# Optimization experiments

Measured on AMD Instinct MI355X. Metric: run time of the kernel, lower is better.

## Reference

```python
import jax, jax.numpy as jnp
import numpy as np

COMMISSION_RATIO = 0.0025
INTEREST_RATE = 0.00008
B, N = 4096, 8192


def setup_inputs() -> dict:
    key = jax.random.key(0)
    k1, k2 = jax.random.split(key)
    w = jax.random.uniform(k1, (B, 1, N), dtype=jnp.float32)
    w = w / jnp.sum(w, axis=-1, keepdims=True)  # portfolio weights sum to 1
    # price relatives close to 1 so log(reward) stays finite
    y = 1.0 + 0.02 * jax.random.normal(k2, (B, N, 1), dtype=jnp.float32)
    return {"w": w, "y": y}


def reference(w, y):
    # reward[b] = w[b] @ y[b]  -> [B,1,1]
    reward = jnp.einsum('bin,bnj->bij', w, y)
    # torch .view(B, 1, N) on contiguous [B, N, 1] == transpose here
    close_price = jnp.swapaxes(y, 1, 2)                     # [B,1,N]
    element_reward = w * close_price                        # [B,1,N]
    # interest: only negative elements contribute
    interest = jnp.sum(jnp.minimum(element_reward, 0.0), axis=2,
                       keepdims=True) * INTEREST_RATE       # [B,1,1]
    future_omega = element_reward / reward                  # [B,1,N]
    wt, wt1 = future_omega[:-1], w[1:]
    pure_pc = 1.0 - jnp.sum(jnp.abs(wt - wt1), axis=-1) * COMMISSION_RATIO  # [B-1,1]
    pure_pc = jnp.concatenate(
        [jnp.ones((1, 1), dtype=pure_pc.dtype), pure_pc], axis=0)  # [B,1]
    pure_pc = pure_pc[:, :, None]                           # [B,1,1]
    reward = reward * pure_pc + interest                    # [B,1,1]

    sr_reward = reward - 1.0
    SR = jnp.mean(sr_reward) / jnp.std(sr_reward, ddof=1)   # torch std is unbiased

    # max drawdown: cumprod of per-step changes, running max, relative dip
    pc = reward.reshape(-1)                                 # [B]
    pv = jnp.cumprod(pc)
    running_max = jax.lax.cummax(pv)
    MDD = jnp.max(1.0 - pv / running_max)

    portfolio_value = jnp.prod(reward, axis=0)              # [1,1]
    loss = -jnp.mean(jnp.log(reward))
    return loss, portfolio_value, SR, MDD
```

## Files before the change

kernel.cpp:

```cpp
#include <hip/hip_runtime.h>
#include <math.h>

#define B_DIM 4096
#define N_DIM 8192
#define K_ROWS 4
#define NBLK (B_DIM / K_ROWS)

__constant__ const float kCommission = 0.0025f;
__constant__ const float kInterest   = 8e-05f;

__global__ __launch_bounds__(256) void fused_reward_kernel(const float* __restrict__ w,
                                                           const float* __restrict__ y,
                                                           float* __restrict__ reward_out) {
    const int s    = blockIdx.x * K_ROWS;
    const int tid  = threadIdx.x;
    const int lane = tid & 63, wave = tid >> 6;
    __shared__ float red[4][3];

    float4 e_prev[8];
    #pragma unroll
    for (int j = 0; j < 8; ++j) e_prev[j] = make_float4(0.f, 0.f, 0.f, 0.f);
    float inv_dprev = 0.f;

    if (s > 0) {
        const float4* wp = (const float4*)(w + (size_t)(s - 1) * N_DIM);
        const float4* yp = (const float4*)(y + (size_t)(s - 1) * N_DIM);
        float4 wv[8], yv[8];
        #pragma unroll
        for (int j = 0; j < 8; ++j) wv[j] = wp[tid + 256 * j];
        #pragma unroll
        for (int j = 0; j < 8; ++j) yv[j] = yp[tid + 256 * j];
        float d = 0.f;
        #pragma unroll
        for (int j = 0; j < 8; ++j) {
            float4 ev;
            ev.x = wv[j].x * yv[j].x; ev.y = wv[j].y * yv[j].y;
            ev.z = wv[j].z * yv[j].z; ev.w = wv[j].w * yv[j].w;
            d += (ev.x + ev.y) + (ev.z + ev.w);
            e_prev[j] = ev;
        }
        #pragma unroll
        for (int off = 32; off; off >>= 1) d += __shfl_down(d, off);
        if (lane == 0) red[wave][0] = d;
        __syncthreads();
        float dot_prev = (red[0][0] + red[1][0]) + (red[2][0] + red[3][0]);
        inv_dprev = 1.0f / dot_prev;
        __syncthreads();
    }

    #pragma unroll 1
    for (int k = 0; k < K_ROWS; ++k) {
        const int r = s + k;
        const float4* wp = (const float4*)(w + (size_t)r * N_DIM);
        const float4* yp = (const float4*)(y + (size_t)r * N_DIM);
        float4 wv[8], yv[8];
        #pragma unroll
        for (int j = 0; j < 8; ++j) wv[j] = wp[tid + 256 * j];
        #pragma unroll
        for (int j = 0; j < 8; ++j) yv[j] = yp[tid + 256 * j];

        float d = 0.f, it = 0.f, cm = 0.f;
        #pragma unroll
        for (int j = 0; j < 8; ++j) {
            float4 ev;
            ev.x = wv[j].x * yv[j].x; ev.y = wv[j].y * yv[j].y;
            ev.z = wv[j].z * yv[j].z; ev.w = wv[j].w * yv[j].w;
            d  += (ev.x + ev.y) + (ev.z + ev.w);
            it += (fminf(ev.x, 0.f) + fminf(ev.y, 0.f)) +
                  (fminf(ev.z, 0.f) + fminf(ev.w, 0.f));
            cm += (fabsf(fmaf(e_prev[j].x, inv_dprev, -wv[j].x)) +
                   fabsf(fmaf(e_prev[j].y, inv_dprev, -wv[j].y))) +
                  (fabsf(fmaf(e_prev[j].z, inv_dprev, -wv[j].z)) +
                   fabsf(fmaf(e_prev[j].w, inv_dprev, -wv[j].w)));
            e_prev[j] = ev;
        }
        #pragma unroll
        for (int off = 32; off; off >>= 1) {
            d  += __shfl_down(d,  off);
            it += __shfl_down(it, off);
            cm += __shfl_down(cm, off);
        }
        if (lane == 0) { red[wave][0] = d; red[wave][1] = it; red[wave][2] = cm; }
        __syncthreads();
        const float dot_r = (red[0][0] + red[1][0]) + (red[2][0] + red[3][0]);
        const float int_r = ((red[0][1] + red[1][1]) + (red[2][1] + red[3][1])) * kInterest;
        const float comm  = (red[0][2] + red[1][2]) + (red[2][2] + red[3][2]);
        const float pc = (r == 0) ? 1.0f : fmaf(-comm, kCommission, 1.0f);
        if (tid == 0) reward_out[r] = dot_r * pc + int_r;
        inv_dprev = 1.0f / dot_r;
        __syncthreads();
    }
}

__global__ __launch_bounds__(1024) void finalize_kernel(const float* __restrict__ reward,
                                                        float* __restrict__ out) {
    const int T = 1024, PER = B_DIM / T;
    const int tid = threadIdx.x;
    const int lane = tid & 63, wave = tid >> 6;

    float r[PER], lc[PER];
    float csum = 0.f;
    #pragma unroll
    for (int j = 0; j < PER; ++j) {
        r[j] = reward[tid * PER + j];
        csum += logf(r[j]);
        lc[j] = csum;
    }

    float v = csum;
    #pragma unroll
    for (int off = 1; off < 64; off <<= 1) {
        float t = __shfl_up(v, off);
        if (lane >= off) v += t;
    }
    __shared__ float wsum[16];
    __shared__ float woff[17];
    if (lane == 63) wsum[wave] = v;
    __syncthreads();
    if (tid == 0) {
        float acc = 0.f;
        for (int i = 0; i < 16; ++i) { woff[i] = acc; acc += wsum[i]; }
        woff[16] = acc;
    }
    __syncthreads();
    float ev = __shfl_up(v, 1);
    if (lane == 0) ev = 0.f;
    const float excl = woff[wave] + ev;
    float S[PER];
    #pragma unroll
    for (int j = 0; j < PER; ++j) S[j] = excl + lc[j];
    const float total_logs = woff[16];

    float rm = -INFINITY;
    float cmax[PER];
    #pragma unroll
    for (int j = 0; j < PER; ++j) { rm = fmaxf(rm, S[j]); cmax[j] = rm; }
    float mv = rm;
    #pragma unroll
    for (int off = 1; off < 64; off <<= 1) {
        float t = __shfl_up(mv, off);
        if (lane >= off) mv = fmaxf(mv, t);
    }
    __shared__ float wmax[16];
    __shared__ float wmoff[16];
    if (lane == 63) wmax[wave] = mv;
    __syncthreads();
    if (tid == 0) {
        float acc = -INFINITY;
        for (int i = 0; i < 16; ++i) { wmoff[i] = acc; acc = fmaxf(acc, wmax[i]); }
    }
    __syncthreads();
    float emv = __shfl_up(mv, 1);
    if (lane == 0) emv = -INFINITY;
    const float mexcl = fmaxf(wmoff[wave], emv);

    float ddmax = 0.f;
    #pragma unroll
    for (int j = 0; j < PER; ++j) {
        float M = fmaxf(mexcl, cmax[j]);
        ddmax = fmaxf(ddmax, 1.0f - expf(S[j] - M));
    }
    #pragma unroll
    for (int off = 32; off; off >>= 1) ddmax = fmaxf(ddmax, __shfl_down(ddmax, off));
    __shared__ float wdd[16];
    if (lane == 0) wdd[wave] = ddmax;

    double sr_ = 0.0;
    #pragma unroll
    for (int j = 0; j < PER; ++j) sr_ += (double)r[j];
    #pragma unroll
    for (int off = 32; off; off >>= 1) sr_ += __shfl_down(sr_, off);
    __shared__ double wsr[16];
    if (lane == 0) wsr[wave] = sr_;
    __syncthreads();
    __shared__ double mean_sh;
    if (tid == 0) {
        double sm = 0.0;
        for (int i = 0; i < 16; ++i) sm += wsr[i];
        mean_sh = sm / (double)B_DIM;
    }
    __syncthreads();
    const double mean = mean_sh;
    double sq = 0.0;
    #pragma unroll
    for (int j = 0; j < PER; ++j) { double dd = (double)r[j] - mean; sq += dd * dd; }
    #pragma unroll
    for (int off = 32; off; off >>= 1) sq += __shfl_down(sq, off);
    __shared__ double wsq[16];
    if (lane == 0) wsq[wave] = sq;
    __syncthreads();

    if (tid == 0) {
        double sm = 0.0;
        for (int i = 0; i < 16; ++i) sm += wsq[i];
        double var = sm / (double)(B_DIM - 1);
        double SR = (mean - 1.0) / sqrt(var);
        float mdd = 0.f;
        for (int i = 0; i < 16; ++i) mdd = fmaxf(mdd, wdd[i]);
        out[0] = -total_logs / (float)B_DIM;
        out[1] = expf(total_logs);
        out[2] = (float)SR;
        out[3] = mdd;
    }
}

extern "C" void kernel_launch(void* const* d_in, const int* in_sizes, int n_in,
                              void* d_out, int out_size, void* d_ws, size_t ws_size,
                              hipStream_t stream) {
    const float* w = (const float*)d_in[0];
    const float* y = (const float*)d_in[1];
    float* out = (float*)d_out;
    float* rew = (float*)d_ws;

    fused_reward_kernel<<<NBLK, 256, 0, stream>>>(w, y, rew);
    finalize_kernel<<<1, 1024, 0, stream>>>(rew, out);
}
```

Before: 58.06 us.

## Prefetch next row during reduction, double-buffer shared reduction, enlarge rows per block

```diff
diff --git a/kernel.cpp b/kernel.cpp
--- a/kernel.cpp
+++ b/kernel.cpp
@@ -3,7 +3,7 @@
 
 #define B_DIM 4096
 #define N_DIM 8192
-#define K_ROWS 4
+#define K_ROWS 16
 #define NBLK (B_DIM / K_ROWS)
 
 __constant__ const float kCommission = 0.0025f;
@@ -15,21 +15,42 @@
     const int s    = blockIdx.x * K_ROWS;
     const int tid  = threadIdx.x;
     const int lane = tid & 63, wave = tid >> 6;
-    __shared__ float red[4][3];
-
+    __shared__ float red[2][4][3];
+
+    const int rp = (s == 0) ? 0 : s - 1;
+    {
+        const float4* wb = (const float4*)(w + (size_t)rp * N_DIM);
+        const float4* yb = (const float4*)(y + (size_t)rp * N_DIM);
+        float4 wv[8], yv[8];
+        #pragma unroll
+        for (int j = 0; j < 8; ++j) wv[j] = wb[tid + 256 * j];
+        #pragma unroll
+        for (int j = 0; j < 8; ++j) yv[j] = yb[tid + 256 * j];
+        float d = 0.f;
+        float4 ep[8];
+        #pragma unroll
+        for (int j = 0; j < 8; ++j) {
+            float4 ev;
+            ev.x = wv[j].x * yv[j].x; ev.y = wv[j].y * yv[j].y;
+            ev.z = wv[j].z * yv[j].z; ev.w = wv[j].w * yv[j].w;
+            d += (ev.x + ev.y) + (ev.z + ev.w);
+            ep[j] = ev;
+        }
+        (void)d; (void)ep;
+    }
+
+    float4 wv[8], yv[8];
     float4 e_prev[8];
-    #pragma unroll
-    for (int j = 0; j < 8; ++j) e_prev[j] = make_float4(0.f, 0.f, 0.f, 0.f);
-    float inv_dprev = 0.f;
-
-    if (s > 0) {
-        const float4* wp = (const float4*)(w + (size_t)(s - 1) * N_DIM);
-        const float4* yp = (const float4*)(y + (size_t)(s - 1) * N_DIM);
-        float4 wv[8], yv[8];
-        #pragma unroll
-        for (int j = 0; j < 8; ++j) wv[j] = wp[tid + 256 * j];
-        #pragma unroll
-        for (int j = 0; j < 8; ++j) yv[j] = yp[tid + 256 * j];
+    float  inv_dprev;
+
+    {
+        const float4* wb = (const float4*)(w + (size_t)rp * N_DIM);
+        const float4* yb = (const float4*)(y + (size_t)rp * N_DIM);
+        #pragma unroll
+        for (int j = 0; j < 8; ++j) wv[j] = wb[tid + 256 * j];
+        #pragma unroll
+        for (int j = 0; j < 8; ++j) yv[j] = yb[tid + 256 * j];
+
         float d = 0.f;
         #pragma unroll
         for (int j = 0; j < 8; ++j) {
@@ -39,25 +60,24 @@
             d += (ev.x + ev.y) + (ev.z + ev.w);
             e_prev[j] = ev;
         }
+
+        const float4* wc = (const float4*)(w + (size_t)s * N_DIM);
+        const float4* yc = (const float4*)(y + (size_t)s * N_DIM);
+        #pragma unroll
+        for (int j = 0; j < 8; ++j) wv[j] = wc[tid + 256 * j];
+        #pragma unroll
+        for (int j = 0; j < 8; ++j) yv[j] = yc[tid + 256 * j];
+
         #pragma unroll
         for (int off = 32; off; off >>= 1) d += __shfl_down(d, off);
-        if (lane == 0) red[wave][0] = d;
+        if (lane == 0) red[0][wave][0] = d;
         __syncthreads();
-        float dot_prev = (red[0][0] + red[1][0]) + (red[2][0] + red[3][0]);
-        inv_dprev = 1.0f / dot_prev;
-        __syncthreads();
+        inv_dprev = 1.0f / ((red[0][0][0] + red[0][1][0]) + (red[0][2][0] + red[0][3][0]));
     }
 
     #pragma unroll 1
     for (int k = 0; k < K_ROWS; ++k) {
         const int r = s + k;
-        const float4* wp = (const float4*)(w + (size_t)r * N_DIM);
-        const float4* yp = (const float4*)(y + (size_t)r * N_DIM);
-        float4 wv[8], yv[8];
-        #pragma unroll
-        for (int j = 0; j < 8; ++j) wv[j] = wp[tid + 256 * j];
-        #pragma unroll
-        for (int j = 0; j < 8; ++j) yv[j] = yp[tid + 256 * j];
 
         float d = 0.f, it = 0.f, cm = 0.f;
         #pragma unroll
@@ -74,21 +94,31 @@
                    fabsf(fmaf(e_prev[j].w, inv_dprev, -wv[j].w)));
             e_prev[j] = ev;
         }
+
+        if (k + 1 < K_ROWS) {
+            const float4* wn = (const float4*)(w + (size_t)(r + 1) * N_DIM);
+            const float4* yn = (const float4*)(y + (size_t)(r + 1) * N_DIM);
+            #pragma unroll
+            for (int j = 0; j < 8; ++j) wv[j] = wn[tid + 256 * j];
+            #pragma unroll
+            for (int j = 0; j < 8; ++j) yv[j] = yn[tid + 256 * j];
+        }
+
         #pragma unroll
         for (int off = 32; off; off >>= 1) {
             d  += __shfl_down(d,  off);
             it += __shfl_down(it, off);
             cm += __shfl_down(cm, off);
         }
-        if (lane == 0) { red[wave][0] = d; red[wave][1] = it; red[wave][2] = cm; }
+        const int pb = (k + 1) & 1;
+        if (lane == 0) { red[pb][wave][0] = d; red[pb][wave][1] = it; red[pb][wave][2] = cm; }
         __syncthreads();
-        const float dot_r = (red[0][0] + red[1][0]) + (red[2][0] + red[3][0]);
-        const float int_r = ((red[0][1] + red[1][1]) + (red[2][1] + red[3][1])) * kInterest;
-        const float comm  = (red[0][2] + red[1][2]) + (red[2][2] + red[3][2]);
+        const float dot_r = (red[pb][0][0] + red[pb][1][0]) + (red[pb][2][0] + red[pb][3][0]);
+        const float int_r = ((red[pb][0][1] + red[pb][1][1]) + (red[pb][2][1] + red[pb][3][1])) * kInterest;
+        const float comm  = (red[pb][0][2] + red[pb][1][2]) + (red[pb][2][2] + red[pb][3][2]);
         const float pc = (r == 0) ? 1.0f : fmaf(-comm, kCommission, 1.0f);
         if (tid == 0) reward_out[r] = dot_r * pc + int_r;
         inv_dprev = 1.0f / dot_r;
-        __syncthreads();
     }
 }
 
```

After: 50.70 us. 1.15x faster.
